# Kernel optimization log

Hardware: AMD Instinct MI355X
Metric: run time of the kernel (lower is better)

Reference implementation:

```python
import jax, jax.numpy as jnp
import numpy as np

NUM_JOINTS = 140
NUM_VERTICES = 13059
NUM_BONES = 28
BATCH = 512


def euler_zyx_to_rot(e):
    """e: [..., 3] Euler angles in (z, y, x) order -> [..., 3, 3] with R = Rz @ Ry @ Rx."""
    z, y, x = e[..., 0], e[..., 1], e[..., 2]
    cx, sx = jnp.cos(x), jnp.sin(x)
    cy, sy = jnp.cos(y), jnp.sin(y)
    cz, sz = jnp.cos(z), jnp.sin(z)
    r00 = cz * cy
    r01 = cz * sy * sx - sz * cx
    r02 = cz * sy * cx + sz * sx
    r10 = sz * cy
    r11 = sz * sy * sx + cz * cx
    r12 = sz * sy * cx - cz * sx
    r20 = -sy
    r21 = cy * sx
    r22 = cy * cx
    R = jnp.stack([r00, r01, r02, r10, r11, r12, r20, r21, r22], axis=-1)
    return R.reshape(e.shape[:-1] + (3, 3))


def _mouse_forward(pose, bone_lengths, center_bone_length, trans, scale,
                   v_template, t_pose_joints, weights, parent, bone_mapper):
    B = pose.shape[0]
    Jn = NUM_JOINTS
    dt = pose.dtype

    bl = jax.nn.sigmoid(bone_lengths / 5.0) * 2.0            # [B, 28]
    R = euler_zyx_to_rot(pose.reshape(B, Jn, 3))             # [B, J, 3, 3]
    Jt = t_pose_joints                                       # [J, 3]

    # bone offsets for joints 1..J-1, scaled per bone_length_mapper
    off = Jt[1:] - Jt[parent[1:]]                            # [J-1, 3]
    blid = bone_mapper[1:]                                   # [J-1]
    bl_g = jnp.where(blid[None, :] >= 0,
                     jnp.take(bl, jnp.maximum(blid, 0), axis=1),
                     jnp.ones((), dt))                       # [B, J-1]
    # joint index 1 (position 0 in the [J-1] arrays) uses center_bone_length
    scale_per = bl_g.at[:, 0].set(center_bone_length[:, 0])
    off_b = off[None] * scale_per[..., None]                 # [B, J-1, 3]

    bottom = jnp.broadcast_to(jnp.array([0., 0., 0., 1.], dt), (B, Jn - 1, 1, 4))
    top = jnp.concatenate([R[:, 1:], off_b[..., None]], axis=-1)   # [B, J-1, 3, 4]
    A = jnp.concatenate([top, bottom], axis=-2)              # [B, J-1, 4, 4] local transforms

    root_t = jnp.broadcast_to(Jt[0], (B, 3))[..., None]      # [B, 3, 1]
    root_top = jnp.concatenate([R[:, 0], root_t], axis=-1)   # [B, 3, 4]
    root_bot = jnp.broadcast_to(jnp.array([0., 0., 0., 1.], dt), (B, 1, 4))
    G0 = jnp.concatenate([root_top, root_bot], axis=-2)      # [B, 4, 4]

    G_init = jnp.zeros((B, Jn, 4, 4), dt).at[:, 0].set(G0)

    def step(G, xs):
        i, p, Ai = xs                                        # Ai: [B, 4, 4]
        Gp = jnp.take(G, p, axis=1)                          # [B, 4, 4]
        Gi = Gp @ Ai
        return G.at[:, i].set(Gi), None

    idx = jnp.arange(1, Jn)
    G, _ = jax.lax.scan(step, G_init, (idx, parent[1:], jnp.swapaxes(A, 0, 1)))

    J_final = G[:, :, :3, 3]                                 # [B, J, 3]

    # subtract rest-pose joint contribution (relative transforms for LBS)
    Jh = jnp.concatenate([jnp.broadcast_to(Jt, (B, Jn, 3)),
                          jnp.zeros((B, Jn, 1), dt)], axis=-1)      # [B, J, 4]
    d = jnp.einsum('bjmn,bjn->bjm', G, Jh)                   # [B, J, 4]
    G_rel = jnp.concatenate([G[..., :3], (G[..., 3] - d)[..., None]], axis=-1)

    # linear blend skinning
    T = jnp.einsum('vj,bjmn->bvmn', weights, G_rel)          # [B, V, 4, 4]
    vh = jnp.concatenate([v_template, jnp.ones((NUM_VERTICES, 1), dt)], axis=-1)
    V = jnp.einsum('bvmn,vn->bvm', T[:, :, :3, :], vh)       # [B, V, 3]

    s = scale[:, 0][:, None, None]
    V = V * s + trans[:, None, :]
    J_out = J_final * s + trans[:, None, :]
    return V, J_out


def setup_inputs() -> dict:
    key = jax.random.key(0)
    ks = jax.random.split(key, 8)
    rng = np.random.default_rng(0)
    parent = np.zeros(NUM_JOINTS, dtype=np.int32)
    for i in range(1, NUM_JOINTS):
        parent[i] = rng.integers(0, i)                       # valid kinematic tree
    bone_mapper = rng.integers(-1, NUM_BONES, size=NUM_JOINTS).astype(np.int32)
    W = jax.random.uniform(ks[6], (NUM_VERTICES, NUM_JOINTS), jnp.float32)
    W = W / jnp.sum(W, axis=1, keepdims=True)                # row-stochastic skinning weights
    return {
        'pose': jax.random.normal(ks[0], (BATCH, NUM_JOINTS * 3), jnp.float32) * 0.2,
        'bone_lengths': jax.random.normal(ks[1], (BATCH, NUM_BONES), jnp.float32),
        'center_bone_length': jax.random.uniform(ks[2], (BATCH, 1), jnp.float32, 0.5, 1.5),
        'trans': jax.random.normal(ks[3], (BATCH, 3), jnp.float32),
        'scale': jax.random.uniform(ks[4], (BATCH, 1), jnp.float32, 0.5, 1.5),
        'v_template': jax.random.normal(ks[5], (NUM_VERTICES, 3), jnp.float32),
        't_pose_joints': jax.random.normal(ks[7], (NUM_JOINTS, 3), jnp.float32),
        'weights': W,
        'parent': jnp.asarray(parent),
        'bone_mapper': jnp.asarray(bone_mapper),
    }


def reference(pose, bone_lengths, center_bone_length, trans, scale,
              v_template, t_pose_joints, weights, parent, bone_mapper):
    return _mouse_forward(pose, bone_lengths, center_bone_length, trans, scale,
                          v_template, t_pose_joints, weights, parent, bone_mapper)
```

## Files before the change

kernel.cpp:

```cpp
#include <hip/hip_runtime.h>
#include <math.h>

#define NJ 140
#define NV 13059
#define NB 512
#define NBONES 28

#define MTILES 103
#define NBLK 12
#define KS 18
#define GRID_GEMM (MTILES*NBLK)

#define APREP_SLOTS (MTILES*KS*512)

typedef _Float16 f16x8 __attribute__((ext_vector_type(8)));
typedef float    f32x4 __attribute__((ext_vector_type(4)));

#define GL16(gp, lp) __builtin_amdgcn_global_load_lds( \
    (const __attribute__((address_space(1))) unsigned int*)(gp), \
    (__attribute__((address_space(3))) unsigned int*)(lp), 16, 0, 0)

__global__ __launch_bounds__(256) void prep_kernel(
    const float* __restrict__ pose,
    const float* __restrict__ bone_lengths,
    const float* __restrict__ cbl,
    const float* __restrict__ trans,
    const float* __restrict__ scale,
    const float* __restrict__ v_template,
    const float* __restrict__ t_pose,
    const int*   __restrict__ parent,
    const int*   __restrict__ bone_mapper,
    const float* __restrict__ weights,
    _Float16* __restrict__ Ap,
    _Float16* __restrict__ Bp,
    float* __restrict__ jout)
{
    const int t = threadIdx.x;

    if (blockIdx.x >= NB) {
        const int id  = blockIdx.x - NB;
        const int mt  = id / KS;
        const int ks  = id - mt*KS;
        const int row = t >> 1;
        const int q   = t & 1;
        const int v   = mt*128 + row;
        const int j0  = ks*8 + q*4;
        const int s   = (row >> 1) & 3;

        f16x8 oA, oB;
        #pragma unroll
        for (int i = 0; i < 8; ++i) { oA[i] = (_Float16)0.f; oB[i] = (_Float16)0.f; }

        if (v < NV && j0 + 3 < NJ) {
            float x = v_template[v*3+0];
            float y = v_template[v*3+1];
            float z = v_template[v*3+2];
            const float4 w4 = *(const float4*)(weights + (size_t)v*NJ + j0);
            oA[0] = (_Float16)(w4.x*x); oA[1] = (_Float16)(w4.x*y);
            oA[2] = (_Float16)(w4.x*z); oA[3] = (_Float16)w4.x;
            oA[4] = (_Float16)(w4.y*x); oA[5] = (_Float16)(w4.y*y);
            oA[6] = (_Float16)(w4.y*z); oA[7] = (_Float16)w4.y;
            oB[0] = (_Float16)(w4.z*x); oB[1] = (_Float16)(w4.z*y);
            oB[2] = (_Float16)(w4.z*z); oB[3] = (_Float16)w4.z;
            oB[4] = (_Float16)(w4.w*x); oB[5] = (_Float16)(w4.w*y);
            oB[6] = (_Float16)(w4.w*z); oB[7] = (_Float16)w4.w;
        }
        const int base = ((2*q) ^ s) & ~1;
        _Float16* dst = Ap + (((size_t)id)*512 + row*4 + base)*8;
        if (s & 1) {
            *(f16x8*)dst       = oB;
            *(f16x8*)(dst + 8) = oA;
        } else {
            *(f16x8*)dst       = oA;
            *(f16x8*)(dst + 8) = oB;
        }
        return;
    }

    __shared__ float M0[NJ][12];
    __shared__ float M1[NJ][12];
    __shared__ int   a0[NJ];
    __shared__ int   a1[NJ];

    const int b = blockIdx.x;

    if (t < NJ) {
        const int j = t;
        float z = pose[b*(NJ*3) + 3*j + 0];
        float y = pose[b*(NJ*3) + 3*j + 1];
        float x = pose[b*(NJ*3) + 3*j + 2];
        float cx = cosf(x), sx = sinf(x);
        float cy = cosf(y), sy = sinf(y);
        float cz = cosf(z), sz = sinf(z);
        float r00 = cz*cy;
        float r01 = cz*sy*sx - sz*cx;
        float r02 = cz*sy*cx + sz*sx;
        float r10 = sz*cy;
        float r11 = sz*sy*sx + cz*cx;
        float r12 = sz*sy*cx - cz*sx;
        float r20 = -sy;
        float r21 = cy*sx;
        float r22 = cy*cx;
        float t0, t1, t2;
        int p = parent[j];
        if (j == 0) {
            t0 = t_pose[0]; t1 = t_pose[1]; t2 = t_pose[2];
        } else {
            float ox = t_pose[3*j+0] - t_pose[3*p+0];
            float oy = t_pose[3*j+1] - t_pose[3*p+1];
            float oz = t_pose[3*j+2] - t_pose[3*p+2];
            float s;
            if (j == 1) {
                s = cbl[b];
            } else {
                int blid = bone_mapper[j];
                if (blid >= 0) {
                    float bv = bone_lengths[b*NBONES + blid];
                    s = 2.0f / (1.0f + expf(-bv*0.2f));
                } else {
                    s = 1.0f;
                }
            }
            t0 = ox*s; t1 = oy*s; t2 = oz*s;
        }
        M0[j][0]=r00; M0[j][1]=r01; M0[j][2]=r02;  M0[j][3]=t0;
        M0[j][4]=r10; M0[j][5]=r11; M0[j][6]=r12;  M0[j][7]=t1;
        M0[j][8]=r20; M0[j][9]=r21; M0[j][10]=r22; M0[j][11]=t2;
        a0[j] = (j == 0) ? -1 : p;
    }
    __syncthreads();

    float* src = &M0[0][0]; float* dst = &M1[0][0];
    int* as = a0; int* ad = a1;
    for (int r = 0; r < 8; ++r) {
        if (t < NJ) {
            int a = as[t];
            const float* Mi = src + t*12;
            float* Do = dst + t*12;
            if (a >= 0) {
                const float* Mp = src + a*12;
                #pragma unroll
                for (int m = 0; m < 3; ++m) {
                    float p0 = Mp[m*4+0], p1 = Mp[m*4+1], p2 = Mp[m*4+2], p3 = Mp[m*4+3];
                    Do[m*4+0] = p0*Mi[0] + p1*Mi[4] + p2*Mi[8];
                    Do[m*4+1] = p0*Mi[1] + p1*Mi[5] + p2*Mi[9];
                    Do[m*4+2] = p0*Mi[2] + p1*Mi[6] + p2*Mi[10];
                    Do[m*4+3] = p0*Mi[3] + p1*Mi[7] + p2*Mi[11] + p3;
                }
                ad[t] = as[a];
            } else {
                #pragma unroll
                for (int e = 0; e < 12; ++e) Do[e] = Mi[e];
                ad[t] = -1;
            }
        }
        __syncthreads();
        float* tf = src; src = dst; dst = tf;
        int* ti = as; as = ad; ad = ti;
    }

    float* grl = dst;
    if (t < NJ) {
        const int j = t;
        const float* G = src + j*12;
        float sb = scale[b];
        float tr0 = trans[b*3+0], tr1 = trans[b*3+1], tr2 = trans[b*3+2];
        float* jo = jout + ((size_t)b*NJ + j)*3;
        jo[0] = G[3]*sb  + tr0;
        jo[1] = G[7]*sb  + tr1;
        jo[2] = G[11]*sb + tr2;
        float jx = t_pose[3*j+0], jy = t_pose[3*j+1], jz = t_pose[3*j+2];
        #pragma unroll
        for (int c = 0; c < 3; ++c) {
            float g0 = G[c*4+0], g1 = G[c*4+1], g2 = G[c*4+2];
            float g3 = G[c*4+3] - (g0*jx + g1*jy + g2*jz);
            grl[j*12 + c*4 + 0] = g0;
            grl[j*12 + c*4 + 1] = g1;
            grl[j*12 + c*4 + 2] = g2;
            grl[j*12 + c*4 + 3] = g3;
        }
    }
    __syncthreads();

    if (t < 216) {
        int c  = t / 72;
        int rr = t - c*72;
        int ks = rr >> 2;
        int ci = rr & 3;
        int nrow = b*3 + c;
        int nbp = nrow >> 7;
        int rl = nrow & 127;
        int j0 = ks*8 + ci*2;
        f16x8 o;
        #pragma unroll
        for (int i = 0; i < 8; ++i) o[i] = (_Float16)0.f;
        if (j0 < NJ) {
            o[0] = (_Float16)grl[j0*12 + c*4 + 0];
            o[1] = (_Float16)grl[j0*12 + c*4 + 1];
            o[2] = (_Float16)grl[j0*12 + c*4 + 2];
            o[3] = (_Float16)grl[j0*12 + c*4 + 3];
        }
        if (j0 + 1 < NJ) {
            o[4] = (_Float16)grl[(j0+1)*12 + c*4 + 0];
            o[5] = (_Float16)grl[(j0+1)*12 + c*4 + 1];
            o[6] = (_Float16)grl[(j0+1)*12 + c*4 + 2];
            o[7] = (_Float16)grl[(j0+1)*12 + c*4 + 3];
        }
        int cs = ci ^ ((rl >> 1) & 3);
        *(f16x8*)(Bp + ((size_t)(nbp*KS + ks)*512 + rl*4 + cs)*8) = o;
    }
}

__global__ __launch_bounds__(256, 4) void gemm_kernel(
    const _Float16* __restrict__ Ap,
    const _Float16* __restrict__ Bp,
    const float* __restrict__ scale,
    const float* __restrict__ trans,
    float* __restrict__ vout)
{
    __shared__ _Float16 sA[3][4096];
    __shared__ _Float16 sB[2][4096];

    const int t    = threadIdx.x;
    const int lane = t & 63;
    const int wid  = t >> 6;
    const int ln   = lane & 15;
    const int kq   = lane >> 4;
    const int wm   = wid & 1;
    const int wn   = wid >> 1;

    const int q8 = GRID_GEMM >> 3;
    const int r8 = GRID_GEMM & 7;
    const int xcd = blockIdx.x & 7;
    const int idx = blockIdx.x >> 3;
    const int wgid = (xcd < r8 ? xcd*(q8+1) : r8*(q8+1) + (xcd-r8)*q8) + idx;

    const int mt = wgid / NBLK;
    const int nb = wgid - mt*NBLK;

    const _Float16* Ag = Ap + (size_t)mt*(KS*4096);
    const _Float16* Bg = Bp + (size_t)nb*(KS*4096);

    const int c1 = wid*64 + lane;
    const int c2 = c1 + 256;
    const int lb1 = wid*512;
    const int lb2 = 2048 + wid*512;

    const int csl = kq ^ ((ln >> 1) & 3);
    const int rA  = wm*64 + ln;
    const int rB  = wn*64 + ln;
    const int afo = rA*32 + csl*8;
    const int bfo = rB*32 + csl*8;

    f32x4 acc[4][4];
    #pragma unroll
    for (int mi = 0; mi < 4; ++mi)
        #pragma unroll
        for (int ni = 0; ni < 4; ++ni)
            acc[mi][ni] = (f32x4){0.f, 0.f, 0.f, 0.f};

    #define STAGE_A(buf, ksv) do { \
        const _Float16* a_ = Ag + (ksv)*4096; \
        GL16(a_ + c1*8, &sA[buf][lb1]); \
        GL16(a_ + c2*8, &sA[buf][lb2]); } while (0)
    #define STAGE_B(buf, ksv) do { \
        const _Float16* b_ = Bg + (ksv)*4096; \
        GL16(b_ + c1*8, &sB[buf][lb1]); \
        GL16(b_ + c2*8, &sB[buf][lb2]); } while (0)

    auto compute = [&](int ba, int bb) {
        f16x8 af[4], bf[4];
        #pragma unroll
        for (int mi = 0; mi < 4; ++mi)
            af[mi] = *(const f16x8*)&sA[ba][afo + mi*512];
        #pragma unroll
        for (int ni = 0; ni < 4; ++ni)
            bf[ni] = *(const f16x8*)&sB[bb][bfo + ni*512];
        __builtin_amdgcn_s_setprio(1);
        #pragma unroll
        for (int mi = 0; mi < 4; ++mi)
            #pragma unroll
            for (int ni = 0; ni < 4; ++ni)
                acc[mi][ni] = __builtin_amdgcn_mfma_f32_16x16x32_f16(
                    af[mi], bf[ni], acc[mi][ni], 0, 0, 0);
        __builtin_amdgcn_s_setprio(0);
    };

    #define STEP(j, bBn, bAn, bAc, bBc) do { \
        asm volatile("s_waitcnt vmcnt(2)" ::: "memory"); \
        __builtin_amdgcn_s_barrier(); \
        STAGE_B(bBn, (j) + 1); \
        STAGE_A(bAn, (j) + 2); \
        compute(bAc, bBc); } while (0)

    STAGE_B(0, 0);
    STAGE_A(0, 0);
    STAGE_A(1, 1);

    #pragma unroll 1
    for (int i = 0; i < 12; i += 6) {
        STEP(i + 0, 1, 2, 0, 0);
        STEP(i + 1, 0, 0, 1, 1);
        STEP(i + 2, 1, 1, 2, 0);
        STEP(i + 3, 0, 2, 0, 1);
        STEP(i + 4, 1, 0, 1, 0);
        STEP(i + 5, 0, 1, 2, 1);
    }
    STEP(12, 1, 2, 0, 0);
    STEP(13, 0, 0, 1, 1);
    STEP(14, 1, 1, 2, 0);
    STEP(15, 0, 2, 0, 1);
    asm volatile("s_waitcnt vmcnt(2)" ::: "memory");
    __builtin_amdgcn_s_barrier();
    STAGE_B(1, 17);
    compute(1, 0);
    asm volatile("s_waitcnt vmcnt(0)" ::: "memory");
    __builtin_amdgcn_s_barrier();
    compute(2, 1);

    #undef STEP
    #undef STAGE_A
    #undef STAGE_B

    long long obase[4]; float es[4], etr[4];
    #pragma unroll
    for (int ni = 0; ni < 4; ++ni) {
        int n  = nb*128 + wn*64 + ni*16 + ln;
        int bq = n / 3;
        int cr = n - bq*3;
        obase[ni] = (long long)bq*(NV*3) + cr;
        es[ni]  = scale[bq];
        etr[ni] = trans[n];
    }
    const int vb = mt*128 + wm*64 + kq*4;
    #pragma unroll
    for (int mi = 0; mi < 4; ++mi) {
        #pragma unroll
        for (int ni = 0; ni < 4; ++ni) {
            #pragma unroll
            for (int r = 0; r < 4; ++r) {
                int vg = vb + mi*16 + r;
                if (vg < NV)
                    vout[obase[ni] + (long long)vg*3] =
                        acc[mi][ni][r]*es[ni] + etr[ni];
            }
        }
    }
}

extern "C" void kernel_launch(void* const* d_in, const int* in_sizes, int n_in,
                              void* d_out, int out_size, void* d_ws, size_t ws_size,
                              hipStream_t stream) {
    const float* pose         = (const float*)d_in[0];
    const float* bone_lengths = (const float*)d_in[1];
    const float* cbl          = (const float*)d_in[2];
    const float* trans        = (const float*)d_in[3];
    const float* scale        = (const float*)d_in[4];
    const float* v_template   = (const float*)d_in[5];
    const float* t_pose       = (const float*)d_in[6];
    const float* weights      = (const float*)d_in[7];
    const int*   parent       = (const int*)d_in[8];
    const int*   bone_mapper  = (const int*)d_in[9];

    float* vout = (float*)d_out;
    float* jout = vout + (size_t)NB*NV*3;

    _Float16* Ap = (_Float16*)d_ws;
    _Float16* Bp = Ap + (size_t)APREP_SLOTS*8;

    prep_kernel<<<NB + MTILES*KS, 256, 0, stream>>>(
        pose, bone_lengths, cbl, trans, scale, v_template, t_pose,
        parent, bone_mapper, weights, Ap, Bp, jout);

    gemm_kernel<<<GRID_GEMM, 256, 0, stream>>>(Ap, Bp, scale, trans, vout);
}
```

Baseline: 166.4 us.

## Stage GEMM epilogue through LDS for coalesced contiguous output stores

The GEMM epilogue used to write each accumulator with a stride of 3 floats across vertices, which gave scattered global stores. It now transposes each half of the output tile through shared memory, reusing the A/B staging buffer. Threads then write contiguous runs of vout per batch item, with scale and trans cached in LDS. This adds barriers, an LDS round trip and a serial loop over batch items in exchange for coalesced writes.

```diff
diff --git a/kernel.cpp b/kernel.cpp
--- a/kernel.cpp
+++ b/kernel.cpp
@@ -218,8 +218,9 @@
     const float* __restrict__ trans,
     float* __restrict__ vout)
 {
-    __shared__ _Float16 sA[3][4096];
-    __shared__ _Float16 sB[2][4096];
+    __shared__ __align__(16) char smem[40960];
+    _Float16 (*sA)[4096] = (_Float16(*)[4096])smem;
+    _Float16 (*sB)[4096] = (_Float16(*)[4096])(smem + 24576);
 
     const int t    = threadIdx.x;
     const int lane = t & 63;
@@ -322,27 +323,56 @@
     #undef STAGE_A
     #undef STAGE_B
 
-    long long obase[4]; float es[4], etr[4];
-    #pragma unroll
-    for (int ni = 0; ni < 4; ++ni) {
-        int n  = nb*128 + wn*64 + ni*16 + ln;
-        int bq = n / 3;
-        int cr = n - bq*3;
-        obase[ni] = (long long)bq*(NV*3) + cr;
-        es[ni]  = scale[bq];
-        etr[ni] = trans[n];
-    }
-    const int vb = mt*128 + wm*64 + kq*4;
-    #pragma unroll
-    for (int mi = 0; mi < 4; ++mi) {
-        #pragma unroll
-        for (int ni = 0; ni < 4; ++ni) {
+    float* Ct    = (float*)smem;
+    float* es_l  = (float*)(smem + 33792);
+    float* etr_l = (float*)(smem + 34304);
+
+    const int vgA = t/3,        crA = t - 3*vgA;
+    const int eB  = t + 256;
+    const int vgB = eB/3,       crB = eB - 3*vgB;
+
+    #pragma unroll 1
+    for (int h = 0; h < 2; ++h) {
+        __syncthreads();
+        if (wn == h) {
             #pragma unroll
-            for (int r = 0; r < 4; ++r) {
-                int vg = vb + mi*16 + r;
-                if (vg < NV)
-                    vout[obase[ni] + (long long)vg*3] =
-                        acc[mi][ni][r]*es[ni] + etr[ni];
+            for (int mi = 0; mi < 4; ++mi)
+                #pragma unroll
+                for (int ni = 0; ni < 4; ++ni)
+                    *(f32x4*)&Ct[(ni*16 + ln)*132 + wm*64 + mi*16 + kq*4] =
+                        acc[mi][ni];
+        }
+        if (h == 0 && t < 128) {
+            int n = nb*128 + t;
+            es_l[t]  = scale[n/3];
+            etr_l[t] = trans[n];
+        }
+        __syncthreads();
+
+        const int n0   = nb*128 + h*64;
+        const int bq0  = n0/3;
+        const int off0 = 3*bq0 - n0;
+        const int bqN  = (n0 + 63)/3 - bq0 + 1;
+
+        #pragma unroll 1
+        for (int bqi = 0; bqi < bqN; ++bqi) {
+            const long long base = (long long)(bq0 + bqi)*(NV*3)
+                                 + (long long)mt*384;
+            {
+                int nrel = off0 + 3*bqi + crA;
+                if (nrel >= 0 && nrel < 64 && mt*128 + vgA < NV) {
+                    int nf = h*64 + nrel;
+                    vout[base + t] =
+                        Ct[nrel*132 + vgA]*es_l[nf] + etr_l[nf];
+                }
+            }
+            if (t < 128) {
+                int nrel = off0 + 3*bqi + crB;
+                if (nrel >= 0 && nrel < 64 && mt*128 + vgB < NV) {
+                    int nf = h*64 + nrel;
+                    vout[base + eB] =
+                        Ct[nrel*132 + vgB]*es_l[nf] + etr_l[nf];
+                }
             }
         }
     }
```

After: 149.4 us. 1.11x faster.
